# Performance work log

Measured on AMD Instinct MI355X. Metric: run time of the kernel, lower is better.

## Reference

```python
import jax, jax.numpy as jnp
import numpy as np

EMBED_DIM = 768
NUM_HEADS = 12
HEAD_DIM = EMBED_DIM // NUM_HEADS
SCALE = HEAD_DIM ** -0.5


def setup_inputs() -> dict:
    key = jax.random.key(0)
    k_x, k_wqkv, k_bqkv, k_wp, k_bp = jax.random.split(key, 5)
    B, N, D = 16, 1024, EMBED_DIM
    x = jax.random.normal(k_x, (B, N, D), dtype=jnp.float32)
    # nn.Linear default init: U(-1/sqrt(fan_in), 1/sqrt(fan_in))
    bound = 1.0 / np.sqrt(D)
    W_qkv = jax.random.uniform(k_wqkv, (D, 3 * D), minval=-bound, maxval=bound, dtype=jnp.float32)
    b_qkv = jax.random.uniform(k_bqkv, (3 * D,), minval=-bound, maxval=bound, dtype=jnp.float32)
    W_proj = jax.random.uniform(k_wp, (D, D), minval=-bound, maxval=bound, dtype=jnp.float32)
    b_proj = jax.random.uniform(k_bp, (D,), minval=-bound, maxval=bound, dtype=jnp.float32)
    return {"x": x, "W_qkv": W_qkv, "b_qkv": b_qkv, "W_proj": W_proj, "b_proj": b_proj}


def reference(x, W_qkv, b_qkv, W_proj, b_proj):
    B, N, D = x.shape
    H, Hd = NUM_HEADS, HEAD_DIM
    qkv = x @ W_qkv + b_qkv                      # [B, N, 3D]
    qkv = qkv.reshape(B, N, 3, H, Hd)
    qkv = jnp.transpose(qkv, (2, 0, 3, 1, 4))    # [3, B, H, N, Hd]
    q, k, v = qkv[0], qkv[1], qkv[2]
    attn = jnp.einsum('bhnd,bhmd->bhnm', q, k) * SCALE  # [B, H, N, N]
    attn = jax.nn.softmax(attn, axis=-1)
    out = jnp.einsum('bhnm,bhmd->bhnd', attn, v)        # [B, H, N, Hd]
    out = jnp.transpose(out, (0, 2, 1, 3)).reshape(B, N, D)
    return out @ W_proj + b_proj
```

## Files before the change

### kernel.cpp

```cpp
#include <hip/hip_runtime.h>
#include <math.h>

typedef _Float16 f16;
typedef _Float16 f16x8 __attribute__((ext_vector_type(8)));
typedef _Float16 f16x4 __attribute__((ext_vector_type(4)));
typedef float    f32x4 __attribute__((ext_vector_type(4)));

#define AS1 __attribute__((address_space(1)))
#define AS3 __attribute__((address_space(3)))

#define QSCALE 0.1803368800f

__device__ __forceinline__ void gload16(const void* g, void* l) {
    __builtin_amdgcn_global_load_lds((const AS1 void*)g, (AS3 void*)l, 16, 0, 0);
}

__global__ __launch_bounds__(256) void cast_x_k(const float* __restrict__ in,
                                                f16* __restrict__ out, int n8)
{
    int i = blockIdx.x * 256 + threadIdx.x;
    const int stride = gridDim.x * 256;
    const float4* in4 = (const float4*)in;
    f16x8* o8 = (f16x8*)out;
    for (; i < n8; i += stride) {
        float4 a = in4[2 * i], b = in4[2 * i + 1];
        f16x8 o = {(f16)a.x, (f16)a.y, (f16)a.z, (f16)a.w,
                   (f16)b.x, (f16)b.y, (f16)b.z, (f16)b.w};
        o8[i] = o;
    }
}

__global__ __launch_bounds__(256) void castT_k(const float* __restrict__ W,
                                               f16* __restrict__ WT, int K, int N)
{
    __shared__ float tile[32][33];
    const int k0 = blockIdx.y * 32, n0 = blockIdx.x * 32;
    const int t = threadIdx.x;
    const int r = t >> 3, cq = t & 7;
    float4 v = *(const float4*)&W[(size_t)(k0 + r) * N + n0 + cq * 4];
    tile[r][cq * 4 + 0] = v.x; tile[r][cq * 4 + 1] = v.y;
    tile[r][cq * 4 + 2] = v.z; tile[r][cq * 4 + 3] = v.w;
    __syncthreads();
    f16x4 pk = {(f16)tile[cq * 4 + 0][r], (f16)tile[cq * 4 + 1][r],
                (f16)tile[cq * 4 + 2][r], (f16)tile[cq * 4 + 3][r]};
    *(f16x4*)&WT[(size_t)(n0 + r) * K + k0 + cq * 4] = pk;
}

#define GEMM_PIPE(APTR, BTPTR, NBN, PERX)                                        \
    __shared__ __align__(16) f16 As[4][256 * 32];                                \
    __shared__ __align__(16) f16 Bs[4][256 * 32];                                \
    const int t = threadIdx.x, lid = t & 63, wid = t >> 6;                       \
    const int wr = wid >> 2, wc = wid & 3;                                       \
    const int g = lid >> 4, cl = lid & 15;                                       \
    const int flat = blockIdx.x;                                                 \
    const int logical = (flat & 7) * (PERX) + (flat >> 3);                       \
    const int bm = logical / (NBN), bn = logical % (NBN);                        \
    f32x4 acc[8][4] = {};                                                        \
    const f16* aG[2]; const f16* bG[2]; int ldsoff[2];                           \
    _Pragma("unroll")                                                            \
    for (int i = 0; i < 2; ++i) {                                                \
        int c_lin = wid * 128 + i * 64 + lid;                                    \
        int row = c_lin >> 2, ch = c_lin & 3;                                    \
        int sch = ch ^ (row & 3);                                                \
        aG[i] = (APTR) + (size_t)(bm * 256 + row) * 768 + sch * 8;               \
        bG[i] = (BTPTR) + (size_t)(bn * 256 + row) * 768 + sch * 8;              \
        ldsoff[i] = (wid * 128 + i * 64) * 8;                                    \
    }                                                                            \
    _Pragma("unroll")                                                            \
    for (int p = 0; p < 3; ++p) {                                                \
        _Pragma("unroll")                                                        \
        for (int i = 0; i < 2; ++i) {                                            \
            gload16(aG[i] + p * 32, &As[p][ldsoff[i]]);                          \
            gload16(bG[i] + p * 32, &Bs[p][ldsoff[i]]);                          \
        }                                                                        \
    }                                                                            \
    for (int kt = 0; kt < 24; ++kt) {                                            \
        int tn = kt + 3; if (tn >= 24) tn -= 24;    \
        _Pragma("unroll")                                                        \
        for (int i = 0; i < 2; ++i) {                                            \
            gload16(aG[i] + tn * 32, &As[tn & 3][ldsoff[i]]);                    \
            gload16(bG[i] + tn * 32, &Bs[tn & 3][ldsoff[i]]);                    \
        }                                                                        \
        asm volatile("s_waitcnt vmcnt(12)" ::: "memory");                        \
        __builtin_amdgcn_s_barrier();                                            \
        const f16* As_ = &As[kt & 3][0];                                         \
        const f16* Bs_ = &Bs[kt & 3][0];                                         \
        const int slotx = (g ^ (cl & 3)) * 8;                                    \
        f16x8 af[8], bf[4];                                                      \
        _Pragma("unroll")                                                        \
        for (int m = 0; m < 8; ++m)                                              \
            af[m] = *(const f16x8*)&As_[(wr * 128 + m * 16 + cl) * 32 + slotx];  \
        _Pragma("unroll")                                                        \
        for (int n = 0; n < 4; ++n)                                              \
            bf[n] = *(const f16x8*)&Bs_[(wc * 64 + n * 16 + cl) * 32 + slotx];   \
        __builtin_amdgcn_s_setprio(1);                                           \
        _Pragma("unroll")                                                        \
        for (int m = 0; m < 8; ++m)                                              \
            _Pragma("unroll")                                                    \
            for (int n = 0; n < 4; ++n)                                          \
                acc[m][n] = __builtin_amdgcn_mfma_f32_16x16x32_f16(              \
                    af[m], bf[n], acc[m][n], 0, 0, 0);                           \
        __builtin_amdgcn_s_setprio(0);                                           \
        __builtin_amdgcn_s_barrier();                                            \
    }

__global__ __launch_bounds__(512, 2)
void qkv_gemm16(const f16* __restrict__ A, const f16* __restrict__ BT,
                const float* __restrict__ bias,
                f16* __restrict__ qws, f16* __restrict__ kws, f16* __restrict__ vt)
{
    GEMM_PIPE(A, BT, 9, 72)
#pragma unroll
    for (int m = 0; m < 8; ++m) {
        int rbase = bm * 256 + wr * 128 + m * 16 + g * 4;
#pragma unroll
        for (int n = 0; n < 4; ++n) {
            int cg = bn * 256 + wc * 64 + n * 16 + cl;
            float bb = bias[cg];
            int which = cg / 768;
            int rem = cg - which * 768;
            int h = rem >> 6, d = rem & 63;
            if (which == 2) {
                int b = rbase >> 10, tok = rbase & 1023;
                f16x4 pk = {(f16)(acc[m][n][0] + bb), (f16)(acc[m][n][1] + bb),
                            (f16)(acc[m][n][2] + bb), (f16)(acc[m][n][3] + bb)};
                *(f16x4*)&vt[((size_t)(b * 12 + h) * 64 + d) * 1024 + tok] = pk;
            } else {
                f16* dst = which ? kws : qws;
                float scl = which ? 1.0f : QSCALE;
#pragma unroll
                for (int r = 0; r < 4; ++r) {
                    int row = rbase + r;
                    int b = row >> 10, tok = row & 1023;
                    dst[((size_t)(b * 12 + h) * 1024 + tok) * 64 + d] =
                        (f16)((acc[m][n][r] + bb) * scl);
                }
            }
        }
    }
}

__global__ __launch_bounds__(512, 2)
void proj_gemm16(const f16* __restrict__ A, const f16* __restrict__ BT,
                 const float* __restrict__ bias, float* __restrict__ C)
{
    GEMM_PIPE(A, BT, 3, 24)
#pragma unroll
    for (int m = 0; m < 8; ++m) {
        int rbase = bm * 256 + wr * 128 + m * 16 + g * 4;
#pragma unroll
        for (int n = 0; n < 4; ++n) {
            int cg = bn * 256 + wc * 64 + n * 16 + cl;
            float bb = bias[cg];
#pragma unroll
            for (int r = 0; r < 4; ++r)
                C[(size_t)(rbase + r) * 768 + cg] = acc[m][n][r] + bb;
        }
    }
}

__global__ __launch_bounds__(256)
void attn16(const f16* __restrict__ Q, const f16* __restrict__ K,
            const f16* __restrict__ VT, f16* __restrict__ AO)
{
    __shared__ __align__(16) f16 kbuf[2][64 * 64];
    __shared__ __align__(16) f16 vbuf[2][64 * 64];
    __shared__ __align__(16) f16 plds[4][16 * 64];

    const int t = threadIdx.x, lid = t & 63, wid = t >> 6;
    const int phys = blockIdx.y * gridDim.x + blockIdx.x;
    const int logical = (phys & 7) * 384 + (phys >> 3);
    const int bh = logical >> 4, qt = logical & 15;

    const int g = lid >> 4, c = lid & 15;
    const size_t hb = (size_t)bh * (1024 * 64);
    const int q0 = qt * 64 + wid * 16;

    const f16* qrow = Q + hb + (size_t)(q0 + c) * 64;
    const f16x8 qf0 = *(const f16x8*)(qrow + g * 8);
    const f16x8 qf1 = *(const f16x8*)(qrow + 32 + g * 8);

    const int srow   = wid * 16 + (lid >> 3);
    const int schunk = ((lid & 7) ^ (lid >> 3)) * 8;

#define ATTN_STAGE(BUF, KT)                                                      \
    {                                                                            \
        const f16* kb_ = K + hb + (size_t)((KT) * 64) * 64;                      \
        const f16* vb_ = VT + hb + (KT) * 64;                                    \
        _Pragma("unroll")                                                        \
        for (int c2 = 0; c2 < 2; ++c2) {                                         \
            gload16(kb_ + (size_t)(srow + c2 * 8) * 64 + schunk,                 \
                    &kbuf[BUF][wid * 1024 + c2 * 512]);                          \
            gload16(vb_ + (size_t)(srow + c2 * 8) * 1024 + schunk,               \
                    &vbuf[BUF][wid * 1024 + c2 * 512]);                          \
        }                                                                        \
    }

    f32x4 o[4] = {};
    float mrun = -INFINITY, lrun = 0.f;
    f16* myp = &plds[wid][0];

    ATTN_STAGE(0, 0)
    __syncthreads();

    int cur = 0;
    for (int kt = 0; kt < 16; ++kt) {
        if (kt < 15) ATTN_STAGE(cur ^ 1, kt + 1)

        const f16* kcur = &kbuf[cur][0];
        const f16* vcur = &vbuf[cur][0];
        const int sw = c & 7;

        f32x4 s[4] = {};
        __builtin_amdgcn_s_setprio(1);
#pragma unroll
        for (int m = 0; m < 4; ++m) {
            const int row = m * 16 + c;
            f16x8 k0f = *(const f16x8*)&kcur[row * 64 + ((g) ^ sw) * 8];
            f16x8 k1f = *(const f16x8*)&kcur[row * 64 + ((4 + g) ^ sw) * 8];
            s[m] = __builtin_amdgcn_mfma_f32_16x16x32_f16(k0f, qf0, s[m], 0, 0, 0);
            s[m] = __builtin_amdgcn_mfma_f32_16x16x32_f16(k1f, qf1, s[m], 0, 0, 0);
        }
        __builtin_amdgcn_s_setprio(0);

        float a0 = fmaxf(fmaxf(s[0][0], s[0][1]), fmaxf(s[0][2], s[0][3]));
        float a1 = fmaxf(fmaxf(s[1][0], s[1][1]), fmaxf(s[1][2], s[1][3]));
        float a2 = fmaxf(fmaxf(s[2][0], s[2][1]), fmaxf(s[2][2], s[2][3]));
        float a3 = fmaxf(fmaxf(s[3][0], s[3][1]), fmaxf(s[3][2], s[3][3]));
        float tmax = fmaxf(fmaxf(a0, a1), fmaxf(a2, a3));
        tmax = fmaxf(tmax, __shfl_xor(tmax, 16));
        tmax = fmaxf(tmax, __shfl_xor(tmax, 32));

        bool keep = __all(tmax - mrun <= 8.0f);
        float mnew = fmaxf(mrun, tmax);
        float mref = keep ? mrun : mnew;

        float ps = 0.f;
        float pe[4][4];
#pragma unroll
        for (int m = 0; m < 4; ++m)
#pragma unroll
            for (int r = 0; r < 4; ++r) {
                float p = __builtin_exp2f(s[m][r] - mref);
                pe[m][r] = p; ps += p;
            }
        ps += __shfl_xor(ps, 16);
        ps += __shfl_xor(ps, 32);

        if (keep) {
            lrun += ps;
        } else {
            float al = __builtin_exp2f(mrun - mnew);
            float al4[4];
#pragma unroll
            for (int r = 0; r < 4; ++r) al4[r] = __shfl(al, g * 4 + r);
#pragma unroll
            for (int n = 0; n < 4; ++n) {
                o[n][0] *= al4[0]; o[n][1] *= al4[1];
                o[n][2] *= al4[2]; o[n][3] *= al4[3];
            }
            lrun = lrun * al + ps;
            mrun = mnew;
        }

#pragma unroll
        for (int m = 0; m < 4; ++m) {
            f16x4 pk = {(f16)pe[m][0], (f16)pe[m][1], (f16)pe[m][2], (f16)pe[m][3]};
            int slot = (2 * m + (g >> 1)) ^ sw;
            *(f16x4*)&myp[c * 64 + slot * 8 + (g & 1) * 4] = pk;
        }
        f16x8 pa[2];
#pragma unroll
        for (int kh = 0; kh < 2; ++kh) {
            int slot = (kh * 4 + g) ^ sw;
            pa[kh] = *(const f16x8*)&myp[c * 64 + slot * 8];
        }
        __builtin_amdgcn_s_setprio(1);
#pragma unroll
        for (int kh = 0; kh < 2; ++kh)
#pragma unroll
            for (int n = 0; n < 4; ++n) {
                const int row = n * 16 + c;
                f16x8 vf = *(const f16x8*)&vcur[row * 64 + ((kh * 4 + g) ^ sw) * 8];
                o[n] = __builtin_amdgcn_mfma_f32_16x16x32_f16(pa[kh], vf, o[n], 0, 0, 0);
            }
        __builtin_amdgcn_s_setprio(0);

        __syncthreads();
        cur ^= 1;
    }

    float il = 1.0f / lrun;
    float il4[4];
#pragma unroll
    for (int r = 0; r < 4; ++r) il4[r] = __shfl(il, g * 4 + r);
    const int b = bh / 12, h = bh - b * 12;
#pragma unroll
    for (int n = 0; n < 4; ++n)
#pragma unroll
        for (int r = 0; r < 4; ++r) {
            int tok = q0 + g * 4 + r;
            AO[(size_t)(b * 1024 + tok) * 768 + h * 64 + n * 16 + c] =
                (f16)(o[n][r] * il4[r]);
        }
}


extern "C" void kernel_launch(void* const* d_in, const int* in_sizes, int n_in,
                              void* d_out, int out_size, void* d_ws, size_t ws_size,
                              hipStream_t stream)
{
    const float* x      = (const float*)d_in[0];
    const float* W_qkv  = (const float*)d_in[1];
    const float* b_qkv  = (const float*)d_in[2];
    const float* W_proj = (const float*)d_in[3];
    const float* b_proj = (const float*)d_in[4];
    float* out = (float*)d_out;

    const size_t per = (size_t)16 * 1024 * 768;
    f16* x16    = (f16*)d_ws;
    f16* wqkvT  = x16 + per;
    f16* wprojT = wqkvT + (size_t)768 * 2304;
    f16* qws    = wprojT + (size_t)768 * 768;
    f16* kws    = qws + per;
    f16* vt     = kws + per;
    f16* aws    = vt + per;

    cast_x_k<<<3072, 256, 0, stream>>>(x, x16, (int)(per / 8));
    castT_k<<<dim3(2304 / 32, 768 / 32), 256, 0, stream>>>(W_qkv, wqkvT, 768, 2304);
    castT_k<<<dim3(768 / 32, 768 / 32), 256, 0, stream>>>(W_proj, wprojT, 768, 768);
    qkv_gemm16<<<576, 512, 0, stream>>>(x16, wqkvT, b_qkv, qws, kws, vt);
    attn16<<<dim3(16, 192), 256, 0, stream>>>(qws, kws, vt, aws);
    proj_gemm16<<<192, 512, 0, stream>>>(aws, wprojT, b_proj, out);
}
```

Before: 369.3 us.

## Switch QKV and projection GEMMs to 128x128 tiles with double-buffered BK=64

Replaces the 256x256, 4-stage, 512-thread GEMM pipeline with 128x128 tiles, a K-step of 64, two LDS buffers and 256 threads per block, using an XOR swizzle over 8 chunks. The grid becomes a plain 2D launch instead of the XCD-interleaved block remap. The aim is more blocks and better CU occupancy, especially for the small projection GEMM that previously launched only 192 blocks. In exchange, operand reuse per tile drops, prefetch depth is reduced and L2 locality from the remap is lost.

```diff
diff --git a/kernel.cpp b/kernel.cpp
--- a/kernel.cpp
+++ b/kernel.cpp
@@ -46,76 +46,77 @@
     *(f16x4*)&WT[(size_t)(n0 + r) * K + k0 + cq * 4] = pk;
 }
 
-#define GEMM_PIPE(APTR, BTPTR, NBN, PERX)                                        \
-    __shared__ __align__(16) f16 As[4][256 * 32];                                \
-    __shared__ __align__(16) f16 Bs[4][256 * 32];                                \
+#define GEMM_MAIN(APTR, BTPTR)                                                   \
+    __shared__ __align__(16) f16 As[2][128 * 64];                                \
+    __shared__ __align__(16) f16 Bs[2][128 * 64];                                \
     const int t = threadIdx.x, lid = t & 63, wid = t >> 6;                       \
-    const int wr = wid >> 2, wc = wid & 3;                                       \
+    const int wr = wid >> 1, wc = wid & 1;                                       \
     const int g = lid >> 4, cl = lid & 15;                                       \
-    const int flat = blockIdx.x;                                                 \
-    const int logical = (flat & 7) * (PERX) + (flat >> 3);                       \
-    const int bm = logical / (NBN), bn = logical % (NBN);                        \
-    f32x4 acc[8][4] = {};                                                        \
-    const f16* aG[2]; const f16* bG[2]; int ldsoff[2];                           \
+    const int bm = blockIdx.y, bn = blockIdx.x;                                  \
+    f32x4 acc[4][4] = {};                                                        \
+    const int srow8 = lid >> 3;                                                  \
+    const int sc = (lid & 7) ^ srow8;                                            \
+    const f16* aG = (APTR) + (size_t)(bm * 128 + wid * 32 + srow8) * 768 + sc * 8;\
+    const f16* bG = (BTPTR) + (size_t)(bn * 128 + wid * 32 + srow8) * 768 + sc * 8;\
+    const int ldsoff = wid * 32 * 64;                                            \
     _Pragma("unroll")                                                            \
-    for (int i = 0; i < 2; ++i) {                                                \
-        int c_lin = wid * 128 + i * 64 + lid;                                    \
-        int row = c_lin >> 2, ch = c_lin & 3;                                    \
-        int sch = ch ^ (row & 3);                                                \
-        aG[i] = (APTR) + (size_t)(bm * 256 + row) * 768 + sch * 8;               \
-        bG[i] = (BTPTR) + (size_t)(bn * 256 + row) * 768 + sch * 8;              \
-        ldsoff[i] = (wid * 128 + i * 64) * 8;                                    \
+    for (int c = 0; c < 4; ++c) {                                                \
+        gload16(aG + c * 8 * 768, &As[0][ldsoff + c * 8 * 64]);                  \
+        gload16(bG + c * 8 * 768, &Bs[0][ldsoff + c * 8 * 64]);                  \
     }                                                                            \
-    _Pragma("unroll")                                                            \
-    for (int p = 0; p < 3; ++p) {                                                \
+    for (int kt = 0; kt < 12; ++kt) {                                            \
+        const int tn = kt + 1;                                                   \
+        if (tn < 12) {                                                           \
+            _Pragma("unroll")                                                    \
+            for (int c = 0; c < 4; ++c) {                                        \
+                gload16(aG + c * 8 * 768 + tn * 64, &As[tn & 1][ldsoff + c * 8 * 64]); \
+                gload16(bG + c * 8 * 768 + tn * 64, &Bs[tn & 1][ldsoff + c * 8 * 64]); \
+            }                                                                    \
+            asm volatile("s_waitcnt vmcnt(8)" ::: "memory");                     \
+        } else {                                                                 \
+            asm volatile("s_waitcnt vmcnt(0)" ::: "memory");                     \
+        }                                                                        \
+        __builtin_amdgcn_s_barrier();                                            \
+        asm volatile("" ::: "memory");                                           \
+        const f16* As_ = &As[kt & 1][0];                                         \
+        const f16* Bs_ = &Bs[kt & 1][0];                                         \
         _Pragma("unroll")                                                        \
-        for (int i = 0; i < 2; ++i) {                                            \
-            gload16(aG[i] + p * 32, &As[p][ldsoff[i]]);                          \
-            gload16(bG[i] + p * 32, &Bs[p][ldsoff[i]]);                          \
+        for (int kh = 0; kh < 2; ++kh) {                                         \
+            f16x8 af[4], bf[4];                                                  \
+            _Pragma("unroll")                                                    \
+            for (int m = 0; m < 4; ++m) {                                        \
+                int row = wr * 64 + m * 16 + cl;                                 \
+                int slot = (kh * 4 + g) ^ (row & 7);                             \
+                af[m] = *(const f16x8*)&As_[row * 64 + slot * 8];                \
+                int col = wc * 64 + m * 16 + cl;                                 \
+                int slotb = (kh * 4 + g) ^ (col & 7);                            \
+                bf[m] = *(const f16x8*)&Bs_[col * 64 + slotb * 8];               \
+            }                                                                    \
+            __builtin_amdgcn_s_setprio(1);                                       \
+            _Pragma("unroll")                                                    \
+            for (int m = 0; m < 4; ++m)                                          \
+                _Pragma("unroll")                                                \
+                for (int n = 0; n < 4; ++n)                                      \
+                    acc[m][n] = __builtin_amdgcn_mfma_f32_16x16x32_f16(          \
+                        af[m], bf[n], acc[m][n], 0, 0, 0);                       \
+            __builtin_amdgcn_s_setprio(0);                                       \
         }                                                                        \
-    }                                                                            \
-    for (int kt = 0; kt < 24; ++kt) {                                            \
-        int tn = kt + 3; if (tn >= 24) tn -= 24;    \
-        _Pragma("unroll")                                                        \
-        for (int i = 0; i < 2; ++i) {                                            \
-            gload16(aG[i] + tn * 32, &As[tn & 3][ldsoff[i]]);                    \
-            gload16(bG[i] + tn * 32, &Bs[tn & 3][ldsoff[i]]);                    \
-        }                                                                        \
-        asm volatile("s_waitcnt vmcnt(12)" ::: "memory");                        \
+        asm volatile("" ::: "memory");                                           \
         __builtin_amdgcn_s_barrier();                                            \
-        const f16* As_ = &As[kt & 3][0];                                         \
-        const f16* Bs_ = &Bs[kt & 3][0];                                         \
-        const int slotx = (g ^ (cl & 3)) * 8;                                    \
-        f16x8 af[8], bf[4];                                                      \
-        _Pragma("unroll")                                                        \
-        for (int m = 0; m < 8; ++m)                                              \
-            af[m] = *(const f16x8*)&As_[(wr * 128 + m * 16 + cl) * 32 + slotx];  \
-        _Pragma("unroll")                                                        \
-        for (int n = 0; n < 4; ++n)                                              \
-            bf[n] = *(const f16x8*)&Bs_[(wc * 64 + n * 16 + cl) * 32 + slotx];   \
-        __builtin_amdgcn_s_setprio(1);                                           \
-        _Pragma("unroll")                                                        \
-        for (int m = 0; m < 8; ++m)                                              \
-            _Pragma("unroll")                                                    \
-            for (int n = 0; n < 4; ++n)                                          \
-                acc[m][n] = __builtin_amdgcn_mfma_f32_16x16x32_f16(              \
-                    af[m], bf[n], acc[m][n], 0, 0, 0);                           \
-        __builtin_amdgcn_s_setprio(0);                                           \
-        __builtin_amdgcn_s_barrier();                                            \
-    }
-
-__global__ __launch_bounds__(512, 2)
+    }
+
+__global__ __launch_bounds__(256)
 void qkv_gemm16(const f16* __restrict__ A, const f16* __restrict__ BT,
                 const float* __restrict__ bias,
                 f16* __restrict__ qws, f16* __restrict__ kws, f16* __restrict__ vt)
 {
-    GEMM_PIPE(A, BT, 9, 72)
-#pragma unroll
-    for (int m = 0; m < 8; ++m) {
-        int rbase = bm * 256 + wr * 128 + m * 16 + g * 4;
+    GEMM_MAIN(A, BT)
+#pragma unroll
+    for (int m = 0; m < 4; ++m) {
+        int rbase = bm * 128 + wr * 64 + m * 16 + g * 4;
 #pragma unroll
         for (int n = 0; n < 4; ++n) {
-            int cg = bn * 256 + wc * 64 + n * 16 + cl;
+            int cg = bn * 128 + wc * 64 + n * 16 + cl;
             float bb = bias[cg];
             int which = cg / 768;
             int rem = cg - which * 768;
@@ -140,17 +141,17 @@
     }
 }
 
-__global__ __launch_bounds__(512, 2)
+__global__ __launch_bounds__(256)
 void proj_gemm16(const f16* __restrict__ A, const f16* __restrict__ BT,
                  const float* __restrict__ bias, float* __restrict__ C)
 {
-    GEMM_PIPE(A, BT, 3, 24)
-#pragma unroll
-    for (int m = 0; m < 8; ++m) {
-        int rbase = bm * 256 + wr * 128 + m * 16 + g * 4;
+    GEMM_MAIN(A, BT)
+#pragma unroll
+    for (int m = 0; m < 4; ++m) {
+        int rbase = bm * 128 + wr * 64 + m * 16 + g * 4;
 #pragma unroll
         for (int n = 0; n < 4; ++n) {
-            int cg = bn * 256 + wc * 64 + n * 16 + cl;
+            int cg = bn * 128 + wc * 64 + n * 16 + cl;
             float bb = bias[cg];
 #pragma unroll
             for (int r = 0; r < 4; ++r)
@@ -329,7 +330,7 @@
     cast_x_k<<<3072, 256, 0, stream>>>(x, x16, (int)(per / 8));
     castT_k<<<dim3(2304 / 32, 768 / 32), 256, 0, stream>>>(W_qkv, wqkvT, 768, 2304);
     castT_k<<<dim3(768 / 32, 768 / 32), 256, 0, stream>>>(W_proj, wprojT, 768, 768);
-    qkv_gemm16<<<576, 512, 0, stream>>>(x16, wqkvT, b_qkv, qws, kws, vt);
+    qkv_gemm16<<<dim3(18, 128), 256, 0, stream>>>(x16, wqkvT, b_qkv, qws, kws, vt);
     attn16<<<dim3(16, 192), 256, 0, stream>>>(qws, kws, vt, aws);
-    proj_gemm16<<<192, 512, 0, stream>>>(aws, wprojT, b_proj, out);
-}
+    proj_gemm16<<<dim3(6, 128), 256, 0, stream>>>(aws, wprojT, b_proj, out);
+}
```

After: 357.1 us. 3.3% less time.
